# Performance work log

Measured on AMD Instinct MI355X. Metric: run time of the kernel, lower is better.

Reference implementation:

```python
import jax, jax.numpy as jnp
import numpy as np

# Arbitrary non-contiguous kernel tap offsets (constructor arg sk_ind)
SK_IND = np.array([-512, -256, -128, -96, -64, -48, -32, -24, -16, -12, -8, -6,
                   -4, -3, -2, -1, 0, 1, 2, 3, 4, 6, 8, 12, 16, 24, 32, 48,
                   64, 96, 128, 256], dtype=np.int32)
IN_CHANNELS = 64
OUT_CHANNELS = 64
BATCH = 16
INPUT_LEN = 4096


def setup_inputs() -> dict:
    key = jax.random.key(0)
    k1, k2 = jax.random.split(key)
    x = jax.random.normal(k1, (BATCH, IN_CHANNELS, INPUT_LEN), dtype=jnp.float32)
    sk_weights = jax.random.normal(k2, (OUT_CHANNELS, IN_CHANNELS, SK_IND.shape[0]), dtype=jnp.float32)
    return {"x": x, "sk_weights": sk_weights}


def reference(x, sk_weights):
    # x: [B, Cin, L]; sk_weights: [Cout, Cin, K]
    B, C, L = x.shape
    low_pad = max(-int(SK_IND.min()), 0)   # zeros consumed by negative taps
    high_pad = max(int(SK_IND.max()), 0)   # zeros consumed by positive taps
    # Original pads zeros AFTER the signal: [x, zeros(high_pad), zeros(low_pad)];
    # negative numpy indices then wrap into the trailing low_pad zeros.
    padded = jnp.concatenate([x, jnp.zeros((B, C, high_pad + low_pad), x.dtype)], axis=-1)
    padded_len = L + high_pad + low_pad
    idx = SK_IND[:, None] + np.arange(L)                 # [K, L], static
    idx = np.where(idx < 0, padded_len + idx, idx)       # emulate numpy negative-index wrap
    gathered = padded[:, :, idx]                          # [B, Cin, K, L]
    # Per-position GEMM: contract over (Cin, K)
    return jnp.einsum('oik,bikl->bol', sk_weights, gathered)  # [B, Cout, L]
```

## Files before the change

### kernel.cpp

```cpp
#include <hip/hip_runtime.h>


#define B_    16
#define CIN   64
#define COUT  64
#define LEN   4096
#define PAD_LO 512
#define PAD_HI 256
#define LPAD  (LEN + PAD_LO + PAD_HI)
#define NTAP  32

typedef float f32x4 __attribute__((ext_vector_type(4)));
typedef short bf16x8_s __attribute__((ext_vector_type(8)));
typedef __bf16 bf16x8_b __attribute__((ext_vector_type(8)));
typedef unsigned short u16x8 __attribute__((ext_vector_type(8)));

template <typename V>
static __device__ inline auto mfma_16x16x32_bf16(V a, V b, f32x4 c, int)
    -> decltype(__builtin_amdgcn_mfma_f32_16x16x32_bf16(a, b, c, 0, 0, 0)) {
  return __builtin_amdgcn_mfma_f32_16x16x32_bf16(a, b, c, 0, 0, 0);
}
template <typename V>
static __device__ inline f32x4 mfma_16x16x32_bf16(V a, V b, f32x4 c, long) {
  return __builtin_amdgcn_mfma_f32_16x16x32_bf16(
      __builtin_bit_cast(bf16x8_b, a), __builtin_bit_cast(bf16x8_b, b), c, 0, 0, 0);
}

static __device__ inline unsigned short f32_to_bf16_rne(float f) {
  unsigned int u = __builtin_bit_cast(unsigned int, f);
  u += 0x7fffu + ((u >> 16) & 1u);
  return (unsigned short)(u >> 16);
}

static __device__ inline void async_copy16(const void* g, void* l) {
  __builtin_amdgcn_global_load_lds((const __attribute__((address_space(1))) unsigned int*)g,
                                   (__attribute__((address_space(3))) unsigned int*)l, 16, 0, 0);
}

__global__ __launch_bounds__(256) void prep_x(const float* __restrict__ x,
                                              unsigned short* __restrict__ xp) {
  __shared__ float tile[64][65];
  const int b = blockIdx.y;
  const int lp0 = blockIdx.x * 64;
  const int tid = threadIdx.x;
  const bool data = (lp0 >= PAD_LO) && (lp0 < PAD_LO + LEN);
  if (data) {
    const int l0 = lp0 - PAD_LO;
#pragma unroll
    for (int it = 0; it < 4; ++it) {
      const int pidx = it * 256 + tid;
      const int il = pidx >> 4;
      const int lq = (pidx & 15) * 4;
      const float4 v = *(const float4*)&x[(size_t)(b * CIN + il) * LEN + l0 + lq];
      tile[lq + 0][il] = v.x;
      tile[lq + 1][il] = v.y;
      tile[lq + 2][il] = v.z;
      tile[lq + 3][il] = v.w;
    }
  }
  __syncthreads();
#pragma unroll
  for (int it = 0; it < 2; ++it) {
    const int pidx = it * 256 + tid;
    const int ll = pidx >> 3;
    const int i8 = (pidx & 7) * 8;
    u16x8 v = {0, 0, 0, 0, 0, 0, 0, 0};
    if (data) {
#pragma unroll
      for (int j = 0; j < 8; ++j) v[j] = f32_to_bf16_rne(tile[ll][i8 + j]);
    }
    *(u16x8*)&xp[(size_t)(b * LPAD + lp0 + ll) * CIN + i8] = v;
  }
}

__global__ __launch_bounds__(256) void prep_w(const float* __restrict__ w,
                                              unsigned short* __restrict__ wf) {
  const int e = blockIdx.x * 256 + threadIdx.x;
  const int j = e & 7;
  const int lane = (e >> 3) & 63;
  const int m = (e >> 9) & 3;
  const int c = (e >> 11) & 1;
  const int t = e >> 12;
  const int q = lane >> 4, r = lane & 15;
  const int o = m * 16 + r;
  const int i = c * 32 + q * 8 + j;
  wf[e] = f32_to_bf16_rne(w[(size_t)(o * CIN + i) * NTAP + t]);
}

__global__ __launch_bounds__(256, 2) void sconv_main(const unsigned short* __restrict__ xp,
                                                     const unsigned short* __restrict__ wf,
                                                     float* __restrict__ out) {
  constexpr int TAP[NTAP] = {-512, -256, -128, -96, -64, -48, -32, -24, -16, -12, -8,
                             -6,   -4,   -3,   -2,  -1,  0,   1,   2,   3,   4,  6,
                             8,    12,   16,   24,  32,  48,  64,  96,  128, 256};
  __shared__ alignas(16) char smem[2][24576];

  const int b = blockIdx.y;
  const int l0 = blockIdx.x * 128;
  const int tid = threadIdx.x;
  const int wave = tid >> 6, lane = tid & 63;
  const int q = lane >> 4, r = lane & 15;
  const int oh = wave & 1, lh = wave >> 1;

  int boff[4];
#pragma unroll
  for (int it = 0; it < 4; ++it) {
    const int s = it * 256 + tid;
    const int row = s >> 3, ch = s & 7;
    boff[it] = (row * 8 + (ch ^ (row & 7))) * 16;
  }

  const char* xbase = (const char*)xp + (size_t)(b * LPAD + l0 + PAD_LO) * (CIN * 2);
  const char* wbase = (const char*)wf;

  auto stage = [&](int t, int p) {
    const char* win = xbase + TAP[t] * (CIN * 2);
#pragma unroll
    for (int it = 0; it < 4; ++it)
      async_copy16(win + boff[it], &smem[p][(it * 256 + wave * 64) * 16]);
    const char* wsrc = wbase + t * 8192;
#pragma unroll
    for (int it = 0; it < 2; ++it)
      async_copy16(wsrc + (it * 256 + wave * 64 + lane) * 16,
                   &smem[p][16384 + (it * 256 + wave * 64) * 16]);
  };

  f32x4 acc[2][4] = {};

  stage(0, 0);

#pragma unroll
  for (int t = 0; t < NTAP; ++t) {
    const int p = t & 1;
    __syncthreads();
    if (t + 1 < NTAP) stage(t + 1, p ^ 1);
    __builtin_amdgcn_sched_barrier(0);
    const char* Bb = smem[p];
    const char* Wb = smem[p] + 16384;
#pragma unroll
    for (int c = 0; c < 2; ++c) {
      bf16x8_s A[2], Bf[4];
#pragma unroll
      for (int m = 0; m < 2; ++m)
        A[m] = *(const bf16x8_s*)(Wb + (c * 256 + (oh * 2 + m) * 64 + lane) * 16);
#pragma unroll
      for (int n = 0; n < 4; ++n) {
        const int row = lh * 64 + n * 16 + r;
        Bf[n] = *(const bf16x8_s*)(Bb + (row * 8 + ((c * 4 + q) ^ (r & 7))) * 16);
      }
#pragma unroll
      for (int m = 0; m < 2; ++m)
#pragma unroll
        for (int n = 0; n < 4; ++n)
          acc[m][n] = mfma_16x16x32_bf16(A[m], Bf[n], acc[m][n], 0);
    }
  }

#pragma unroll
  for (int m = 0; m < 2; ++m)
#pragma unroll
    for (int n = 0; n < 4; ++n)
#pragma unroll
      for (int d = 0; d < 4; ++d) {
        const int o = oh * 32 + m * 16 + q * 4 + d;
        const int l = l0 + lh * 64 + n * 16 + r;
        out[(size_t)(b * COUT + o) * LEN + l] = acc[m][n][d];
      }
}

extern "C" void kernel_launch(void* const* d_in, const int* in_sizes, int n_in,
                              void* d_out, int out_size, void* d_ws, size_t ws_size,
                              hipStream_t stream) {
  const float* x = (const float*)d_in[0];
  const float* w = (const float*)d_in[1];
  float* out = (float*)d_out;

  unsigned short* xp = (unsigned short*)d_ws;
  unsigned short* wfp = xp + (size_t)B_ * LPAD * CIN;

  prep_x<<<dim3(LPAD / 64, B_), 256, 0, stream>>>(x, xp);
  prep_w<<<dim3((NTAP * 2 * 4 * 64 * 8) / 256), 256, 0, stream>>>(w, wfp);
  sconv_main<<<dim3(LEN / 128, B_), 256, 0, stream>>>(xp, wfp, out);
}
```

Before: 94.05 us.

## Triple-buffer activation windows with explicit vmcnt waits and remap block order

Splits shared memory into a three-deep ring for activation tiles and a two-deep ring for weights, so activation loads are issued two taps ahead. It replaces __syncthreads with explicit s_waitcnt on outstanding vector-memory loads plus s_barrier. It also flattens the grid and remaps block IDs so that consecutive blocks cover different batches, which is meant to spread traffic across memory channels and caches. Shared memory per block grows from 48KB to 64KB, which may affect occupancy, and the hand-encoded waitcnt values must match the actual count of in-flight loads.

```diff
diff --git a/kernel.cpp b/kernel.cpp
--- a/kernel.cpp
+++ b/kernel.cpp
@@ -93,10 +93,12 @@
   constexpr int TAP[NTAP] = {-512, -256, -128, -96, -64, -48, -32, -24, -16, -12, -8,
                              -6,   -4,   -3,   -2,  -1,  0,   1,   2,   3,   4,  6,
                              8,    12,   16,   24,  32,  48,  64,  96,  128, 256};
-  __shared__ alignas(16) char smem[2][24576];
+  __shared__ alignas(16) char bbuf[3][16384];
+  __shared__ alignas(16) char wbuf[2][8192];
 
-  const int b = blockIdx.y;
-  const int l0 = blockIdx.x * 128;
+  const int id = blockIdx.x;
+  const int b = (id & 7) * 2 + (id >> 8);
+  const int l0 = ((id >> 3) & 31) * 128;
   const int tid = threadIdx.x;
   const int wave = tid >> 6, lane = tid & 63;
   const int q = lane >> 4, r = lane & 15;
@@ -113,30 +115,39 @@
   const char* xbase = (const char*)xp + (size_t)(b * LPAD + l0 + PAD_LO) * (CIN * 2);
   const char* wbase = (const char*)wf;
 
-  auto stage = [&](int t, int p) {
-    const char* win = xbase + TAP[t] * (CIN * 2);
-#pragma unroll
-    for (int it = 0; it < 4; ++it)
-      async_copy16(win + boff[it], &smem[p][(it * 256 + wave * 64) * 16]);
+  auto stageW = [&](int t, int p) {
     const char* wsrc = wbase + t * 8192;
 #pragma unroll
     for (int it = 0; it < 2; ++it)
       async_copy16(wsrc + (it * 256 + wave * 64 + lane) * 16,
-                   &smem[p][16384 + (it * 256 + wave * 64) * 16]);
+                   &wbuf[p][(it * 256 + wave * 64) * 16]);
+  };
+  auto stageB = [&](int t, int p) {
+    const char* win = xbase + TAP[t] * (CIN * 2);
+#pragma unroll
+    for (int it = 0; it < 4; ++it)
+      async_copy16(win + boff[it], &bbuf[p][(it * 256 + wave * 64) * 16]);
   };
 
   f32x4 acc[2][4] = {};
 
-  stage(0, 0);
+  stageW(0, 0);
+  stageB(0, 0);
+  stageB(1, 1);
 
 #pragma unroll
   for (int t = 0; t < NTAP; ++t) {
-    const int p = t & 1;
-    __syncthreads();
-    if (t + 1 < NTAP) stage(t + 1, p ^ 1);
     __builtin_amdgcn_sched_barrier(0);
-    const char* Bb = smem[p];
-    const char* Wb = smem[p] + 16384;
+    if (t == NTAP - 1) __builtin_amdgcn_s_waitcnt(0x0F70);
+    else               __builtin_amdgcn_s_waitcnt(0x0F74);
+    __builtin_amdgcn_s_barrier();
+    __builtin_amdgcn_sched_barrier(0);
+    if (t + 1 < NTAP) stageW(t + 1, (t + 1) & 1);
+    if (t + 2 < NTAP) stageB(t + 2, (t + 2) % 3);
+    __builtin_amdgcn_sched_barrier(0);
+
+    const char* Bb = bbuf[t % 3];
+    const char* Wb = wbuf[t & 1];
 #pragma unroll
     for (int c = 0; c < 2; ++c) {
       bf16x8_s A[2], Bf[4];
@@ -180,5 +191,5 @@
 
   prep_x<<<dim3(LPAD / 64, B_), 256, 0, stream>>>(x, xp);
   prep_w<<<dim3((NTAP * 2 * 4 * 64 * 8) / 256), 256, 0, stream>>>(w, wfp);
-  sconv_main<<<dim3(LEN / 128, B_), 256, 0, stream>>>(xp, wfp, out);
+  sconv_main<<<dim3(16 * 32), 256, 0, stream>>>(xp, wfp, out);
 }
```

Measured after the change: 97.42 us. 1.04x slower.

## Use sliding ring buffer of input rows shared across taps, larger output tile

Applied to the files above, without the earlier changes.

The main kernel now computes a 256-position by 64-channel output tile per block, with each wave covering all 64 output channels. It keeps a 512-row ring buffer of bf16 input rows in LDS, and for each tap it only streams in the rows newly needed as the window slides to the next tap offset. Previously every tap reloaded a full 128-row window. This cuts global/L2 traffic for x and doubles the weight reuse per MFMA. The cost is 80KB of LDS per block and more accumulator registers, which lowers occupancy, and the grid shrinks to 256 blocks.

```diff
diff --git a/kernel.cpp b/kernel.cpp
--- a/kernel.cpp
+++ b/kernel.cpp
@@ -93,63 +93,71 @@
   constexpr int TAP[NTAP] = {-512, -256, -128, -96, -64, -48, -32, -24, -16, -12, -8,
                              -6,   -4,   -3,   -2,  -1,  0,   1,   2,   3,   4,  6,
                              8,    12,   16,   24,  32,  48,  64,  96,  128, 256};
-  __shared__ alignas(16) char smem[2][24576];
+  __shared__ alignas(16) char smem[81920];
 
-  const int b = blockIdx.y;
-  const int l0 = blockIdx.x * 128;
+  const int id = blockIdx.x;
+  const int b = id >> 4;
+  const int l0 = (id & 15) * 256;
+  const int lb = l0 + PAD_LO;
   const int tid = threadIdx.x;
-  const int wave = tid >> 6, lane = tid & 63;
+  const int wv = tid >> 6, lane = tid & 63;
   const int q = lane >> 4, r = lane & 15;
-  const int oh = wave & 1, lh = wave >> 1;
 
-  int boff[4];
-#pragma unroll
-  for (int it = 0; it < 4; ++it) {
-    const int s = it * 256 + tid;
-    const int row = s >> 3, ch = s & 7;
-    boff[it] = (row * 8 + (ch ^ (row & 7))) * 16;
-  }
-
-  const char* xbase = (const char*)xp + (size_t)(b * LPAD + l0 + PAD_LO) * (CIN * 2);
+  const char* xbase = (const char*)xp + ((size_t)b * LPAD + lb) * (CIN * 2);
   const char* wbase = (const char*)wf;
 
-  auto stage = [&](int t, int p) {
-    const char* win = xbase + TAP[t] * (CIN * 2);
-#pragma unroll
-    for (int it = 0; it < 4; ++it)
-      async_copy16(win + boff[it], &smem[p][(it * 256 + wave * 64) * 16]);
-    const char* wsrc = wbase + t * 8192;
+  auto stageW = [&](int t) {
+    const char* src = wbase + t * 8192;
+    char* dst = smem + (t & 1) * 8192;
 #pragma unroll
     for (int it = 0; it < 2; ++it)
-      async_copy16(wsrc + (it * 256 + wave * 64 + lane) * 16,
-                   &smem[p][16384 + (it * 256 + wave * 64) * 16]);
+      async_copy16(src + (it * 256 + wv * 64 + lane) * 16,
+                   dst + (it * 256 + wv * 64) * 16);
+  };
+  auto stageB = [&](int a0, int ng) {
+    for (int g = wv; g < ng; g += 4) {
+      const int ra = a0 + g * 8 + (lane >> 3);
+      const int ch = (lane & 7) ^ (ra & 7);
+      const int sb = (lb + a0 + g * 8) & 511;
+      async_copy16(xbase + (ptrdiff_t)ra * 128 + ch * 16, smem + 16384 + sb * 128);
+    }
   };
 
-  f32x4 acc[2][4] = {};
+  f32x4 acc[4][4] = {};
 
-  stage(0, 0);
+  stageW(0);
+  stageB(-512, 32);
 
 #pragma unroll
   for (int t = 0; t < NTAP; ++t) {
-    const int p = t & 1;
     __syncthreads();
-    if (t + 1 < NTAP) stage(t + 1, p ^ 1);
+    if (t + 1 < NTAP) {
+      stageW(t + 1);
+      const int dstart = TAP[t] + 256;
+      const int dend = TAP[t + 1] + 256;
+      const int a0 = dstart & ~7;
+      stageB(a0, (dend - a0 + 7) >> 3);
+    }
     __builtin_amdgcn_sched_barrier(0);
-    const char* Bb = smem[p];
-    const char* Wb = smem[p] + 16384;
+
+    const int e = (TAP[t] + r) & 7;
+    int baddr[4];
+#pragma unroll
+    for (int n = 0; n < 4; ++n) {
+      const int slot = (lb + TAP[t] + wv * 64 + 16 * n + r) & 511;
+      baddr[n] = 16384 + slot * 128 + ((q ^ e) << 4);
+    }
 #pragma unroll
     for (int c = 0; c < 2; ++c) {
-      bf16x8_s A[2], Bf[4];
+      bf16x8_s A[4], Bf[4];
 #pragma unroll
-      for (int m = 0; m < 2; ++m)
-        A[m] = *(const bf16x8_s*)(Wb + (c * 256 + (oh * 2 + m) * 64 + lane) * 16);
+      for (int m = 0; m < 4; ++m)
+        A[m] = *(const bf16x8_s*)(smem + (t & 1) * 8192 + (c * 4 + m) * 1024 + lane * 16);
 #pragma unroll
-      for (int n = 0; n < 4; ++n) {
-        const int row = lh * 64 + n * 16 + r;
-        Bf[n] = *(const bf16x8_s*)(Bb + (row * 8 + ((c * 4 + q) ^ (r & 7))) * 16);
-      }
+      for (int n = 0; n < 4; ++n)
+        Bf[n] = *(const bf16x8_s*)(smem + (baddr[n] ^ (c << 6)));
 #pragma unroll
-      for (int m = 0; m < 2; ++m)
+      for (int m = 0; m < 4; ++m)
 #pragma unroll
         for (int n = 0; n < 4; ++n)
           acc[m][n] = mfma_16x16x32_bf16(A[m], Bf[n], acc[m][n], 0);
@@ -157,14 +165,14 @@
   }
 
 #pragma unroll
-  for (int m = 0; m < 2; ++m)
+  for (int m = 0; m < 4; ++m)
 #pragma unroll
     for (int n = 0; n < 4; ++n)
 #pragma unroll
       for (int d = 0; d < 4; ++d) {
-        const int o = oh * 32 + m * 16 + q * 4 + d;
-        const int l = l0 + lh * 64 + n * 16 + r;
-        out[(size_t)(b * COUT + o) * LEN + l] = acc[m][n][d];
+        const int o = 16 * m + 4 * q + d;
+        const int l = l0 + wv * 64 + 16 * n + r;
+        out[((size_t)b * COUT + o) * LEN + l] = acc[m][n][d];
       }
 }
 
@@ -180,5 +188,5 @@
 
   prep_x<<<dim3(LPAD / 64, B_), 256, 0, stream>>>(x, xp);
   prep_w<<<dim3((NTAP * 2 * 4 * 64 * 8) / 256), 256, 0, stream>>>(w, wfp);
-  sconv_main<<<dim3(LEN / 128, B_), 256, 0, stream>>>(xp, wfp, out);
+  sconv_main<<<dim3(B_ * 16), 256, 0, stream>>>(xp, wfp, out);
 }
```

Result: no change. 93.97 us (-0.1%).
